# Kernel tuning notes

Hardware: AMD Instinct MI355X
Metric: run time of the kernel (lower is better)

Reference implementation:

```python
import jax, jax.numpy as jnp
import numpy as np

C = 16          # n_comp per axis
G = 300         # grid resolution per axis
N = 2_000_000   # number of sampled points


def setup_inputs() -> dict:
    key = jax.random.key(0)
    k1, k2, k3 = jax.random.split(key, 3)
    # normalized coordinates in [-1, 1] (grid_sample convention)
    xyz = jax.random.uniform(k1, (N, 3), minval=-1.0, maxval=1.0, dtype=jnp.float32)
    planes = 0.1 * jax.random.normal(k2, (3, C, G, G), dtype=jnp.float32)  # (axis, C, H, W)
    lines = 0.1 * jax.random.normal(k3, (3, C, G), dtype=jnp.float32)      # (axis, C, G)
    return {"xyz": xyz, "planes": planes, "lines": lines}


def _lerp_idx(coord, size):
    # align_corners=True mapping: [-1,1] -> [0, size-1]
    x = (coord + 1.0) * 0.5 * (size - 1)
    x0 = jnp.clip(jnp.floor(x), 0, size - 1).astype(jnp.int32)
    x1 = jnp.minimum(x0 + 1, size - 1)
    w = x - x0.astype(x.dtype)
    return x0, x1, w


def _sample_plane(plane, gx, gy):
    # plane: (C, H, W); gx, gy: (N,) in [-1,1]; grid x indexes W, y indexes H
    H, W = plane.shape[-2:]
    x0, x1, wx = _lerp_idx(gx, W)
    y0, y1, wy = _lerp_idx(gy, H)
    v00 = plane[:, y0, x0]  # (C, N)
    v01 = plane[:, y0, x1]
    v10 = plane[:, y1, x0]
    v11 = plane[:, y1, x1]
    return (v00 * (1 - wx) + v01 * wx) * (1 - wy) + (v10 * (1 - wx) + v11 * wx) * wy


def _sample_line(line, g):
    # line: (C, G); g: (N,) in [-1,1]; width dim of original (G,1) grid is size 1 -> ignored
    Gs = line.shape[-1]
    y0, y1, wy = _lerp_idx(g, Gs)
    return line[:, y0] * (1 - wy) + line[:, y1] * wy  # (C, N)


def reference(xyz, planes, lines):
    # matMode[i] = axes != i; plane i sampled at (x=xyz[id_0], y=xyz[id_1])
    matMode = ((1, 2), (0, 2), (0, 1))
    feats = []
    for i in range(3):
        a, b = matMode[i]
        p = _sample_plane(planes[i], xyz[:, a], xyz[:, b])  # (C, N)
        l = _sample_line(lines[i], xyz[:, i])               # (C, N)
        feats.append(p * l)
    return jnp.concatenate(feats, axis=0)  # (3*C, N)
```

## Files before the change

kernel.cpp:

```cpp
#include <hip/hip_runtime.h>

#define CC 16
#define GG 300

typedef unsigned int  u32;
typedef unsigned short u16;

__device__ __forceinline__ float bf_lo(u32 u) { union { u32 i; float f; } v; v.i = u << 16;          return v.f; }
__device__ __forceinline__ float bf_hi(u32 u) { union { u32 i; float f; } v; v.i = u & 0xffff0000u;  return v.f; }
__device__ __forceinline__ u16 f2bf(float f) {
    union { float f; u32 i; } v; v.f = f;
    u32 r = v.i + 0x7fffu + ((v.i >> 16) & 1u);
    return (u16)(r >> 16);
}

__global__ void transpose_planes_k(const float* __restrict__ src, u32* __restrict__ dst) {
    int tid = blockIdx.x * blockDim.x + threadIdx.x;
    const int total = 3 * GG * GG;
    if (tid >= total) return;
    int x = tid % GG;
    int y = (tid / GG) % GG;
    int i = tid / (GG * GG);
    u32 packed[8];
#pragma unroll
    for (int h = 0; h < 8; ++h) {
        float a = src[((size_t)(i * CC + 2 * h)     * GG + y) * GG + x];
        float b = src[((size_t)(i * CC + 2 * h + 1) * GG + y) * GG + x];
        packed[h] = (u32)f2bf(a) | ((u32)f2bf(b) << 16);
    }
    uint4* d = (uint4*)(dst + (size_t)tid * 8);
    d[0] = make_uint4(packed[0], packed[1], packed[2], packed[3]);
    d[1] = make_uint4(packed[4], packed[5], packed[6], packed[7]);
}

__global__ void transpose_lines_k(const float* __restrict__ src, u32* __restrict__ dst) {
    int tid = blockIdx.x * blockDim.x + threadIdx.x;
    const int total = 3 * GG;
    if (tid >= total) return;
    int g = tid % GG;
    int i = tid / GG;
    u32 packed[8];
#pragma unroll
    for (int h = 0; h < 8; ++h) {
        float a = src[(size_t)(i * CC + 2 * h)     * GG + g];
        float b = src[(size_t)(i * CC + 2 * h + 1) * GG + g];
        packed[h] = (u32)f2bf(a) | ((u32)f2bf(b) << 16);
    }
    uint4* d = (uint4*)(dst + (size_t)tid * 8);
    d[0] = make_uint4(packed[0], packed[1], packed[2], packed[3]);
    d[1] = make_uint4(packed[4], packed[5], packed[6], packed[7]);
}

__device__ __forceinline__ float bilerp(float v00, float v01, float v10, float v11,
                                        float wx, float wy) {
    float ox = 1.0f - wx, oy = 1.0f - wy;
    return (v00 * ox + v01 * wx) * oy + (v10 * ox + v11 * wx) * wy;
}

__global__ __launch_bounds__(256) void sample_plane_k(
    const float* __restrict__ xyz,
    const u32* __restrict__ planesT,
    const u32* __restrict__ linesT,
    float* __restrict__ out, int N, int nbPer)
{
    const int plane = blockIdx.x / nbPer;
    const int n = (blockIdx.x % nbPer) * 256 + threadIdx.x;
    if (n >= N) return;

    float crd[3];
    crd[0] = __builtin_nontemporal_load(xyz + 3 * (size_t)n + 0);
    crd[1] = __builtin_nontemporal_load(xyz + 3 * (size_t)n + 1);
    crd[2] = __builtin_nontemporal_load(xyz + 3 * (size_t)n + 2);

    int i0[3], i1[3];
    float w[3];
#pragma unroll
    for (int k = 0; k < 3; ++k) {
        float xk = (crd[k] + 1.0f) * 0.5f * (float)(GG - 1);
        float xf = floorf(xk);
        xf = fminf(fmaxf(xf, 0.0f), (float)(GG - 1));
        i0[k] = (int)xf;
        i1[k] = min(i0[k] + 1, GG - 1);
        w[k] = xk - xf;
    }

    const int mata[3] = {1, 0, 0};
    const int matb[3] = {2, 2, 1};
    const int a = mata[plane];
    const int b = matb[plane];

    const int xa0 = i0[a], xa1 = i1[a];
    const int yb0 = i0[b], yb1 = i1[b];
    const float wx = w[a], wy = w[b], wz = w[plane];
    const float oz = 1.0f - wz;

    const u32* pb = planesT + (size_t)plane * (GG * GG * 8);
    const uint4* c00 = (const uint4*)(pb + (size_t)(yb0 * GG + xa0) * 8);
    const uint4* c01 = (const uint4*)(pb + (size_t)(yb0 * GG + xa1) * 8);
    const uint4* c10 = (const uint4*)(pb + (size_t)(yb1 * GG + xa0) * 8);
    const uint4* c11 = (const uint4*)(pb + (size_t)(yb1 * GG + xa1) * 8);
    const uint4* lp0 = (const uint4*)(linesT + ((size_t)plane * GG + i0[plane]) * 8);
    const uint4* lp1 = (const uint4*)(linesT + ((size_t)plane * GG + i1[plane]) * 8);

    uint4 A00 = c00[0], B00 = c00[1];
    uint4 A01 = c01[0], B01 = c01[1];
    uint4 A10 = c10[0], B10 = c10[1];
    uint4 A11 = c11[0], B11 = c11[1];
    uint4 AL0 = lp0[0], BL0 = lp0[1];
    uint4 AL1 = lp1[0], BL1 = lp1[1];

    u32 r00[8] = {A00.x, A00.y, A00.z, A00.w, B00.x, B00.y, B00.z, B00.w};
    u32 r01[8] = {A01.x, A01.y, A01.z, A01.w, B01.x, B01.y, B01.z, B01.w};
    u32 r10[8] = {A10.x, A10.y, A10.z, A10.w, B10.x, B10.y, B10.z, B10.w};
    u32 r11[8] = {A11.x, A11.y, A11.z, A11.w, B11.x, B11.y, B11.z, B11.w};
    u32 rl0[8] = {AL0.x, AL0.y, AL0.z, AL0.w, BL0.x, BL0.y, BL0.z, BL0.w};
    u32 rl1[8] = {AL1.x, AL1.y, AL1.z, AL1.w, BL1.x, BL1.y, BL1.z, BL1.w};

#pragma unroll
    for (int u = 0; u < 8; ++u) {
        float p0 = bilerp(bf_lo(r00[u]), bf_lo(r01[u]), bf_lo(r10[u]), bf_lo(r11[u]), wx, wy);
        float p1 = bilerp(bf_hi(r00[u]), bf_hi(r01[u]), bf_hi(r10[u]), bf_hi(r11[u]), wx, wy);
        float l0 = bf_lo(rl0[u]) * oz + bf_lo(rl1[u]) * wz;
        float l1 = bf_hi(rl0[u]) * oz + bf_hi(rl1[u]) * wz;
        size_t row = (size_t)(plane * CC + 2 * u);
        __builtin_nontemporal_store(p0 * l0, &out[row * (size_t)N + n]);
        __builtin_nontemporal_store(p1 * l1, &out[(row + 1) * (size_t)N + n]);
    }
}

__global__ __launch_bounds__(256) void sample_fallback_k(
    const float* __restrict__ xyz,
    const float* __restrict__ planes,
    const float* __restrict__ lines,
    float* __restrict__ out, int N)
{
    int n = blockIdx.x * blockDim.x + threadIdx.x;
    if (n >= N) return;

    float crd[3];
    crd[0] = xyz[3 * n + 0];
    crd[1] = xyz[3 * n + 1];
    crd[2] = xyz[3 * n + 2];

    int i0[3], i1[3];
    float w[3];
#pragma unroll
    for (int k = 0; k < 3; ++k) {
        float xk = (crd[k] + 1.0f) * 0.5f * (float)(GG - 1);
        float xf = floorf(xk);
        xf = fminf(fmaxf(xf, 0.0f), (float)(GG - 1));
        i0[k] = (int)xf;
        i1[k] = min(i0[k] + 1, GG - 1);
        w[k] = xk - xf;
    }

    const int mata[3] = {1, 0, 0};
    const int matb[3] = {2, 2, 1};

    for (int i = 0; i < 3; ++i) {
        const int xa0 = i0[mata[i]], xa1 = i1[mata[i]];
        const int yb0 = i0[matb[i]], yb1 = i1[matb[i]];
        const float wx = w[mata[i]], wy = w[matb[i]], wz = w[i];
        const float oz = 1.0f - wz;
        const float* pb = planes + (size_t)i * (CC * GG * GG);
        const float* lb = lines + (size_t)i * (CC * GG);
        for (int c = 0; c < CC; ++c) {
            const float* pc = pb + (size_t)c * (GG * GG);
            float p = bilerp(pc[yb0 * GG + xa0], pc[yb0 * GG + xa1],
                             pc[yb1 * GG + xa0], pc[yb1 * GG + xa1], wx, wy);
            float l = lb[c * GG + i0[i]] * oz + lb[c * GG + i1[i]] * wz;
            out[(size_t)(i * CC + c) * (size_t)N + n] = p * l;
        }
    }
}

extern "C" void kernel_launch(void* const* d_in, const int* in_sizes, int n_in,
                              void* d_out, int out_size, void* d_ws, size_t ws_size,
                              hipStream_t stream) {
    const float* xyz    = (const float*)d_in[0];
    const float* planes = (const float*)d_in[1];
    const float* lines  = (const float*)d_in[2];
    float* out = (float*)d_out;
    const int N = in_sizes[0] / 3;

    const size_t planesT_u32 = (size_t)3 * GG * GG * 8;
    const size_t linesT_u32  = (size_t)3 * GG * 8;
    const size_t need = (planesT_u32 + linesT_u32) * sizeof(u32);

    if (ws_size >= need) {
        u32* planesT = (u32*)d_ws;
        u32* linesT  = planesT + planesT_u32;
        {
            int total = 3 * GG * GG;
            transpose_planes_k<<<(total + 255) / 256, 256, 0, stream>>>(planes, planesT);
        }
        {
            int total = 3 * GG;
            transpose_lines_k<<<(total + 255) / 256, 256, 0, stream>>>(lines, linesT);
        }
        int nbPer = (N + 255) / 256;
        sample_plane_k<<<3 * nbPer, 256, 0, stream>>>(xyz, planesT, linesT, out, N, nbPer);
    } else {
        sample_fallback_k<<<(N + 255) / 256, 256, 0, stream>>>(xyz, planes, lines, out, N);
    }
}
```

Baseline: 542.9 us.

## Split each point's channels across two threads and stage line table in LDS

```diff
diff --git a/kernel.cpp b/kernel.cpp
--- a/kernel.cpp
+++ b/kernel.cpp
@@ -57,74 +57,83 @@
     return (v00 * ox + v01 * wx) * oy + (v10 * ox + v11 * wx) * wy;
 }
 
-__global__ __launch_bounds__(256) void sample_plane_k(
+__global__ __launch_bounds__(256) void sample_pair_k(
     const float* __restrict__ xyz,
     const u32* __restrict__ planesT,
     const u32* __restrict__ linesT,
     float* __restrict__ out, int N, int nbPer)
 {
+    __shared__ uint4 lineLds[GG * 2];
+
     const int plane = blockIdx.x / nbPer;
-    const int n = (blockIdx.x % nbPer) * 256 + threadIdx.x;
-    if (n >= N) return;
-
-    float crd[3];
-    crd[0] = __builtin_nontemporal_load(xyz + 3 * (size_t)n + 0);
-    crd[1] = __builtin_nontemporal_load(xyz + 3 * (size_t)n + 1);
-    crd[2] = __builtin_nontemporal_load(xyz + 3 * (size_t)n + 2);
-
-    int i0[3], i1[3];
-    float w[3];
-#pragma unroll
-    for (int k = 0; k < 3; ++k) {
-        float xk = (crd[k] + 1.0f) * 0.5f * (float)(GG - 1);
-        float xf = floorf(xk);
-        xf = fminf(fmaxf(xf, 0.0f), (float)(GG - 1));
-        i0[k] = (int)xf;
-        i1[k] = min(i0[k] + 1, GG - 1);
-        w[k] = xk - xf;
-    }
-
-    const int mata[3] = {1, 0, 0};
-    const int matb[3] = {2, 2, 1};
-    const int a = mata[plane];
-    const int b = matb[plane];
-
-    const int xa0 = i0[a], xa1 = i1[a];
-    const int yb0 = i0[b], yb1 = i1[b];
-    const float wx = w[a], wy = w[b], wz = w[plane];
-    const float oz = 1.0f - wz;
+
+    const uint4* lsrc = (const uint4*)(linesT + (size_t)plane * (GG * 8));
+    for (int idx = threadIdx.x; idx < GG * 2; idx += 256)
+        lineLds[idx] = lsrc[idx];
+    __syncthreads();
+
+    const int t = (blockIdx.x % nbPer) * 256 + (int)threadIdx.x;
+    const int p = t >> 1;
+    const int h = t & 1;
+    if (p >= N) return;
+
+    const float cx = __builtin_nontemporal_load(xyz + 3 * (size_t)p + 0);
+    const float cy = __builtin_nontemporal_load(xyz + 3 * (size_t)p + 1);
+    const float cz = __builtin_nontemporal_load(xyz + 3 * (size_t)p + 2);
+
+    int i0x, i1x, i0y, i1y, i0z, i1z;
+    float wxa, wya, wza;
+    {
+        float xk = (cx + 1.0f) * 0.5f * (float)(GG - 1);
+        float xf = fminf(fmaxf(floorf(xk), 0.0f), (float)(GG - 1));
+        i0x = (int)xf; i1x = min(i0x + 1, GG - 1); wxa = xk - xf;
+    }
+    {
+        float xk = (cy + 1.0f) * 0.5f * (float)(GG - 1);
+        float xf = fminf(fmaxf(floorf(xk), 0.0f), (float)(GG - 1));
+        i0y = (int)xf; i1y = min(i0y + 1, GG - 1); wya = xk - xf;
+    }
+    {
+        float xk = (cz + 1.0f) * 0.5f * (float)(GG - 1);
+        float xf = fminf(fmaxf(floorf(xk), 0.0f), (float)(GG - 1));
+        i0z = (int)xf; i1z = min(i0z + 1, GG - 1); wza = xk - xf;
+    }
+
+    const int   xa0 = (plane == 0) ? i0y : i0x;
+    const int   xa1 = (plane == 0) ? i1y : i1x;
+    const int   yb0 = (plane == 2) ? i0y : i0z;
+    const int   yb1 = (plane == 2) ? i1y : i1z;
+    const float wx  = (plane == 0) ? wya : wxa;
+    const float wy  = (plane == 2) ? wya : wza;
+    const int   l0i = (plane == 0) ? i0x : ((plane == 1) ? i0y : i0z);
+    const int   l1i = (plane == 0) ? i1x : ((plane == 1) ? i1y : i1z);
+    const float wz  = (plane == 0) ? wxa : ((plane == 1) ? wya : wza);
+    const float oz  = 1.0f - wz;
 
     const u32* pb = planesT + (size_t)plane * (GG * GG * 8);
-    const uint4* c00 = (const uint4*)(pb + (size_t)(yb0 * GG + xa0) * 8);
-    const uint4* c01 = (const uint4*)(pb + (size_t)(yb0 * GG + xa1) * 8);
-    const uint4* c10 = (const uint4*)(pb + (size_t)(yb1 * GG + xa0) * 8);
-    const uint4* c11 = (const uint4*)(pb + (size_t)(yb1 * GG + xa1) * 8);
-    const uint4* lp0 = (const uint4*)(linesT + ((size_t)plane * GG + i0[plane]) * 8);
-    const uint4* lp1 = (const uint4*)(linesT + ((size_t)plane * GG + i1[plane]) * 8);
-
-    uint4 A00 = c00[0], B00 = c00[1];
-    uint4 A01 = c01[0], B01 = c01[1];
-    uint4 A10 = c10[0], B10 = c10[1];
-    uint4 A11 = c11[0], B11 = c11[1];
-    uint4 AL0 = lp0[0], BL0 = lp0[1];
-    uint4 AL1 = lp1[0], BL1 = lp1[1];
-
-    u32 r00[8] = {A00.x, A00.y, A00.z, A00.w, B00.x, B00.y, B00.z, B00.w};
-    u32 r01[8] = {A01.x, A01.y, A01.z, A01.w, B01.x, B01.y, B01.z, B01.w};
-    u32 r10[8] = {A10.x, A10.y, A10.z, A10.w, B10.x, B10.y, B10.z, B10.w};
-    u32 r11[8] = {A11.x, A11.y, A11.z, A11.w, B11.x, B11.y, B11.z, B11.w};
-    u32 rl0[8] = {AL0.x, AL0.y, AL0.z, AL0.w, BL0.x, BL0.y, BL0.z, BL0.w};
-    u32 rl1[8] = {AL1.x, AL1.y, AL1.z, AL1.w, BL1.x, BL1.y, BL1.z, BL1.w};
-
-#pragma unroll
-    for (int u = 0; u < 8; ++u) {
-        float p0 = bilerp(bf_lo(r00[u]), bf_lo(r01[u]), bf_lo(r10[u]), bf_lo(r11[u]), wx, wy);
-        float p1 = bilerp(bf_hi(r00[u]), bf_hi(r01[u]), bf_hi(r10[u]), bf_hi(r11[u]), wx, wy);
-        float l0 = bf_lo(rl0[u]) * oz + bf_lo(rl1[u]) * wz;
-        float l1 = bf_hi(rl0[u]) * oz + bf_hi(rl1[u]) * wz;
-        size_t row = (size_t)(plane * CC + 2 * u);
-        __builtin_nontemporal_store(p0 * l0, &out[row * (size_t)N + n]);
-        __builtin_nontemporal_store(p1 * l1, &out[(row + 1) * (size_t)N + n]);
+    const uint4 q00 = *((const uint4*)(pb + (size_t)(yb0 * GG + xa0) * 8) + h);
+    const uint4 q01 = *((const uint4*)(pb + (size_t)(yb0 * GG + xa1) * 8) + h);
+    const uint4 q10 = *((const uint4*)(pb + (size_t)(yb1 * GG + xa0) * 8) + h);
+    const uint4 q11 = *((const uint4*)(pb + (size_t)(yb1 * GG + xa1) * 8) + h);
+    const uint4 ql0 = lineLds[l0i * 2 + h];
+    const uint4 ql1 = lineLds[l1i * 2 + h];
+
+    const u32 a00[4] = {q00.x, q00.y, q00.z, q00.w};
+    const u32 a01[4] = {q01.x, q01.y, q01.z, q01.w};
+    const u32 a10[4] = {q10.x, q10.y, q10.z, q10.w};
+    const u32 a11[4] = {q11.x, q11.y, q11.z, q11.w};
+    const u32 al0[4] = {ql0.x, ql0.y, ql0.z, ql0.w};
+    const u32 al1[4] = {ql1.x, ql1.y, ql1.z, ql1.w};
+
+    const size_t rowbase = (size_t)(plane * CC + 8 * h);
+#pragma unroll
+    for (int u = 0; u < 4; ++u) {
+        float plo = bilerp(bf_lo(a00[u]), bf_lo(a01[u]), bf_lo(a10[u]), bf_lo(a11[u]), wx, wy);
+        float phi = bilerp(bf_hi(a00[u]), bf_hi(a01[u]), bf_hi(a10[u]), bf_hi(a11[u]), wx, wy);
+        float llo = bf_lo(al0[u]) * oz + bf_lo(al1[u]) * wz;
+        float lhi = bf_hi(al0[u]) * oz + bf_hi(al1[u]) * wz;
+        __builtin_nontemporal_store(plo * llo, &out[(rowbase + 2 * u)     * (size_t)N + p]);
+        __builtin_nontemporal_store(phi * lhi, &out[(rowbase + 2 * u + 1) * (size_t)N + p]);
     }
 }
 
@@ -198,8 +207,8 @@
             int total = 3 * GG;
             transpose_lines_k<<<(total + 255) / 256, 256, 0, stream>>>(lines, linesT);
         }
-        int nbPer = (N + 255) / 256;
-        sample_plane_k<<<3 * nbPer, 256, 0, stream>>>(xyz, planesT, linesT, out, N, nbPer);
+        int nbPer = (int)(((size_t)2 * N + 255) / 256);
+        sample_pair_k<<<3 * nbPer, 256, 0, stream>>>(xyz, planesT, linesT, out, N, nbPer);
     } else {
         sample_fallback_k<<<(N + 255) / 256, 256, 0, stream>>>(xyz, planes, lines, out, N);
     }
```

Result: faster. 512.8 us (-5.6%).
